# Performance work log

Hardware: AMD Instinct MI355X
Metric: run time of the kernel (lower is better)

The kernel has to match this reference:

```python
import jax, jax.numpy as jnp
import numpy as np

NUM_HEADS = 8
NUM_LEVELS = 4
NUM_POINTS = 4


def setup_inputs() -> dict:
    key = jax.random.key(0)
    kq, kp, kv, k1, k2, k3, k4 = jax.random.split(key, 7)
    B, Q, C = 4, 4096, 256
    M, L, P = NUM_HEADS, NUM_LEVELS, NUM_POINTS
    shapes_np = np.array([[128, 128], [64, 64], [32, 32], [16, 16]], dtype=np.int32)
    sizes = shapes_np[:, 0] * shapes_np[:, 1]
    N = int(sizes.sum())  # 21760
    level_index = jnp.asarray(np.concatenate([[0], np.cumsum(sizes)[:-1]]).astype(np.int32))
    q = jax.random.normal(kq, (B, Q, C), jnp.float32)
    p = jax.random.uniform(kp, (B, Q, L, 2), jnp.float32)  # normalized ref points
    v = jax.random.normal(kv, (B, N, C), jnp.float32)
    # proj_offset bias: radial grid init from reset_parameters()
    t = np.arange(M, dtype=np.float32) * (2.0 * np.pi / M)
    grid = np.stack([np.cos(t), np.sin(t)], -1)
    grid = grid / np.abs(grid).max(-1, keepdims=True)
    grid = np.tile(grid[:, None, None, :], (1, L, P, 1)) * np.arange(1, P + 1, dtype=np.float32)[None, None, :, None]
    b_off = jnp.asarray(grid.reshape(-1))
    s = 1.0 / np.sqrt(C).astype(np.float32)
    W_off = jax.random.normal(k1, (C, M * L * P * 2), jnp.float32) * 0.01
    W_attn = jax.random.normal(k2, (C, M * L * P), jnp.float32) * s
    b_attn = jnp.zeros((M * L * P,), jnp.float32)
    W_val = jax.random.normal(k3, (C, C), jnp.float32) * s
    b_val = jnp.zeros((C,), jnp.float32)
    W_out = jax.random.normal(k4, (C, C), jnp.float32) * s
    b_out = jnp.zeros((C,), jnp.float32)
    return {"q": q, "p": p, "v": v, "shapes": jnp.asarray(shapes_np), "level_index": level_index,
            "W_off": W_off, "b_off": b_off, "W_attn": W_attn, "b_attn": b_attn,
            "W_val": W_val, "b_val": b_val, "W_out": W_out, "b_out": b_out}


def _ms_deform_attn(q, p, v, shapes, level_index, W_off, b_off, W_attn, b_attn, W_val, b_val, W_out, b_out):
    B, Q, C = q.shape
    M, L, P = NUM_HEADS, NUM_LEVELS, NUM_POINTS
    D = C // M
    N = v.shape[1]
    # value projection -> [B, M, N, D] (head-major for gather)
    v_p = (v @ W_val + b_val).reshape(B, N, M, D).transpose(0, 2, 1, 3)
    # attention weights, softmax over L*P (classic MSDeformAttn kernel contract)
    attn = jax.nn.softmax((q @ W_attn + b_attn).reshape(B, Q, M, L * P), axis=-1)
    attn = attn.reshape(B, Q, M, L, P)
    # sampling locations (P==2 reference-point branch)
    off = (q @ W_off + b_off).reshape(B, Q, M, L, P, 2)
    norm = jnp.stack([shapes[:, 1], shapes[:, 0]], -1).astype(jnp.float32)  # (W, H) per level
    loc = p[:, :, None, :, None, :] + off / norm[None, None, None, :, None, :]  # [B,Q,M,L,P,2]

    out = jnp.zeros((B, M, Q, D), jnp.float32)
    for l in range(L):
        Hf = shapes[l, 0].astype(jnp.float32)
        Wf = shapes[l, 1].astype(jnp.float32)
        Hi = shapes[l, 0]
        Wi = shapes[l, 1]
        base = level_index[l]
        # grid_sample(align_corners=False) convention: pixel = loc*size - 0.5
        x = loc[:, :, :, l, :, 0] * Wf - 0.5  # [B,Q,M,P]
        y = loc[:, :, :, l, :, 1] * Hf - 0.5
        x0 = jnp.floor(x)
        y0 = jnp.floor(y)
        lx, ly = x - x0, y - y0
        x0i = x0.astype(jnp.int32)
        y0i = y0.astype(jnp.int32)

        def corner(xi, yi, w):
            valid = (xi >= 0) & (xi < Wi) & (yi >= 0) & (yi < Hi)
            idx = base + jnp.clip(yi, 0, Hi - 1) * Wi + jnp.clip(xi, 0, Wi - 1)  # [B,Q,M,P]
            idx = idx.transpose(0, 2, 1, 3).reshape(B, M, Q * P)
            g = jnp.take_along_axis(v_p, idx[..., None], axis=2).reshape(B, M, Q, P, D)
            wv = (w * valid.astype(w.dtype)).transpose(0, 2, 1, 3)[..., None]  # [B,M,Q,P,1]
            return g * wv

        samp = (corner(x0i, y0i, (1 - lx) * (1 - ly))
                + corner(x0i + 1, y0i, lx * (1 - ly))
                + corner(x0i, y0i + 1, (1 - lx) * ly)
                + corner(x0i + 1, y0i + 1, lx * ly))  # [B,M,Q,P,D]
        a_l = attn[:, :, :, l, :].transpose(0, 2, 1, 3)  # [B,M,Q,P]
        out = out + jnp.einsum('bmqpd,bmqp->bmqd', samp, a_l)

    out = out.transpose(0, 2, 1, 3).reshape(B, Q, M * D)
    return out @ W_out + b_out


def reference(q, p, v, shapes, level_index, W_off, b_off, W_attn, b_attn, W_val, b_val, W_out, b_out):
    return _ms_deform_attn(q, p, v, shapes, level_index, W_off, b_off, W_attn, b_attn, W_val, b_val, W_out, b_out)
```

## Files before the change

### kernel.cpp

```cpp
#include <hip/hip_runtime.h>
#include <cstddef>

#define BB 4
#define QQ 4096
#define MM 8
#define NN 21760

typedef __bf16 bf16_8 __attribute__((ext_vector_type(8)));
typedef __bf16 bf16_4 __attribute__((ext_vector_type(4)));
typedef float  floatx4 __attribute__((ext_vector_type(4)));

__global__ __launch_bounds__(256) void prep_weights(
    const float* __restrict__ Wv, const float* __restrict__ Wa,
    const float* __restrict__ Wo, const float* __restrict__ Wu,
    const float* __restrict__ ba, const float* __restrict__ bo,
    __bf16* __restrict__ Wt, float* __restrict__ biasq)
{
    const int gid = blockIdx.x * 256 + threadIdx.x;
    if (gid < 65536) {
        const int n = gid >> 8, k = gid & 255;
        Wt[gid] = (__bf16)Wv[k * 256 + n];
    } else if (gid < 163840) {
        const int o = gid - 65536;
        const int n = o >> 8, k = o & 255;
        Wt[gid] = (__bf16)(n < 128 ? Wa[k * 128 + n] : Wo[k * 256 + (n - 128)]);
    } else if (gid < 229376) {
        const int o = gid - 163840;
        const int n = o >> 8, k = o & 255;
        Wt[gid] = (__bf16)Wu[k * 256 + n];
    } else if (gid < 229760) {
        const int j = gid - 229376;
        biasq[j] = (j < 128) ? ba[j] : bo[j - 128];
    }
}

template<typename AT, int NCOLS, int MODE>
__global__ __launch_bounds__(256) void gemm_k64(
    const AT* __restrict__ A,
    const __bf16* __restrict__ Bt,
    const float* __restrict__ bias,
    void* __restrict__ Cout,
    int tokens, int ldc)
{
    constexpr int NJ  = NCOLS / 64;
    constexpr int BCH = NCOLS / 32;

    const int z    = blockIdx.z;
    const int row0 = blockIdx.y * 64;
    const AT* Ab = A + (size_t)z * tokens * 256;

    __shared__ __bf16 As[64][68];
    __shared__ __bf16 Bs[NCOLS][68];

    const int tid  = threadIdx.x;
    const int lane = tid & 63;
    const int wave = tid >> 6;
    const int quad = lane >> 4;
    const int l16  = lane & 15;
    const int wave_n = wave * (NCOLS / 4);

    floatx4 acc[4][NJ] = {};

    for (int k0 = 0; k0 < 256; k0 += 64) {
        float4 a4[4];
        bf16_8 a8[2];
        if (sizeof(AT) == 4) {
            const float* Af = (const float*)Ab;
            #pragma unroll
            for (int c = 0; c < 4; ++c) {
                const int cid = c * 256 + tid;
                const int r   = cid >> 4;
                const int kc  = (cid & 15) * 4;
                a4[c] = *(const float4*)(Af + (size_t)(row0 + r) * 256 + k0 + kc);
            }
        } else {
            const __bf16* Ah = (const __bf16*)Ab;
            #pragma unroll
            for (int c = 0; c < 2; ++c) {
                const int cid = c * 256 + tid;
                const int r   = cid >> 3;
                const int kc  = (cid & 7) * 8;
                a8[c] = *(const bf16_8*)(Ah + (size_t)(row0 + r) * 256 + k0 + kc);
            }
        }
        bf16_8 b8[BCH];
        #pragma unroll
        for (int c = 0; c < BCH; ++c) {
            const int cid = c * 256 + tid;
            const int n   = cid >> 3;
            const int kc  = (cid & 7) * 8;
            b8[c] = *(const bf16_8*)(Bt + (size_t)n * 256 + k0 + kc);
        }
        if (sizeof(AT) == 4) {
            #pragma unroll
            for (int c = 0; c < 4; ++c) {
                const int cid = c * 256 + tid;
                const int r   = cid >> 4;
                const int kc  = (cid & 15) * 4;
                bf16_4 w;
                w[0] = (__bf16)a4[c].x; w[1] = (__bf16)a4[c].y;
                w[2] = (__bf16)a4[c].z; w[3] = (__bf16)a4[c].w;
                *(bf16_4*)&As[r][kc] = w;
            }
        } else {
            #pragma unroll
            for (int c = 0; c < 2; ++c) {
                const int cid = c * 256 + tid;
                const int r   = cid >> 3;
                const int kc  = (cid & 7) * 8;
                *(bf16_8*)&As[r][kc] = a8[c];
            }
        }
        #pragma unroll
        for (int c = 0; c < BCH; ++c) {
            const int cid = c * 256 + tid;
            const int n   = cid >> 3;
            const int kc  = (cid & 7) * 8;
            *(bf16_8*)&Bs[n][kc] = b8[c];
        }
        __syncthreads();
        #pragma unroll
        for (int h = 0; h < 2; ++h) {
            bf16_8 af[4], bfr[NJ];
            #pragma unroll
            for (int i = 0; i < 4; ++i)
                af[i] = *(const bf16_8*)&As[i * 16 + l16][h * 32 + quad * 8];
            #pragma unroll
            for (int j = 0; j < NJ; ++j)
                bfr[j] = *(const bf16_8*)&Bs[wave_n + j * 16 + l16][h * 32 + quad * 8];
            #pragma unroll
            for (int i = 0; i < 4; ++i)
                #pragma unroll
                for (int j = 0; j < NJ; ++j)
                    acc[i][j] = __builtin_amdgcn_mfma_f32_16x16x32_bf16(af[i], bfr[j], acc[i][j], 0, 0, 0);
        }
        __syncthreads();
    }

    #pragma unroll
    for (int j = 0; j < NJ; ++j) {
        const int col = wave_n + j * 16 + l16;
        const float bc = bias[col];
        #pragma unroll
        for (int i = 0; i < 4; ++i) {
            #pragma unroll
            for (int r = 0; r < 4; ++r) {
                const int row = row0 + i * 16 + quad * 4 + r;
                const float val = acc[i][j][r] + bc;
                if (MODE == 0) {
                    ((float*)Cout)[((size_t)z * tokens + row) * ldc + col] = val;
                } else {
                    const int m = col >> 5, dd = col & 31;
                    ((__bf16*)Cout)[(((size_t)z * 8 + m) * NN + row) * 32 + dd] = (__bf16)val;
                }
            }
        }
    }
}

__device__ __forceinline__ float bflo(unsigned u) { return __uint_as_float(u << 16); }
__device__ __forceinline__ float bfhi(unsigned u) { return __uint_as_float(u & 0xffff0000u); }

__global__ __launch_bounds__(512) void sampler(
    const __bf16* __restrict__ vp,
    const float* __restrict__ gqp,
    const float* __restrict__ pref,
    __bf16* __restrict__ mid)
{
    const int t    = threadIdx.x;
    const int m    = t >> 6;
    const int lane = t & 63;
    const int s    = lane >> 2;
    const int c    = lane & 3;
    const int l    = s >> 2;
    const int bq   = blockIdx.x;
    const int b    = bq >> 12;

    const int   Hi = 128 >> l;
    const float Hf = (float)Hi;
    const int   base = (l == 0) ? 0 : (l == 1) ? 16384 : (l == 2) ? 20480 : 21504;

    const float logit = gqp[(size_t)bq * 384 + m * 16 + s];
    const float e = __expf(logit);
    float sum = e;
    #pragma unroll
    for (int k = 4; k < 64; k <<= 1) sum += __shfl_xor(sum, k, 64);
    const float a = e * __builtin_amdgcn_rcpf(sum);

    const float2 off = *(const float2*)(gqp + (size_t)bq * 384 + 128 + (m * 16 + s) * 2);
    const float2 pr  = *(const float2*)(pref + (size_t)bq * 8 + l * 2);

    const float x = fmaf(pr.x, Hf, off.x - 0.5f);
    const float y = fmaf(pr.y, Hf, off.y - 0.5f);
    const float x0f = floorf(x), y0f = floorf(y);
    const float lx = x - x0f, ly = y - y0f;
    const int x0 = (int)x0f, y0 = (int)y0f;
    const int cx0 = min(max(x0, 0), Hi - 1), cx1 = min(max(x0 + 1, 0), Hi - 1);
    const int cy0 = min(max(y0, 0), Hi - 1), cy1 = min(max(y0 + 1, 0), Hi - 1);
    const bool vx0 = (x0 >= 0) && (x0 < Hi), vx1 = (x0 + 1 >= 0) && (x0 + 1 < Hi);
    const bool vy0 = (y0 >= 0) && (y0 < Hi), vy1 = (y0 + 1 >= 0) && (y0 + 1 < Hi);
    const float w00 = a * (1.f - lx) * (1.f - ly) * ((vx0 && vy0) ? 1.f : 0.f);
    const float w10 = a * lx * (1.f - ly) * ((vx1 && vy0) ? 1.f : 0.f);
    const float w01 = a * (1.f - lx) * ly * ((vx0 && vy1) ? 1.f : 0.f);
    const float w11 = a * lx * ly * ((vx1 && vy1) ? 1.f : 0.f);

    const __bf16* vbase = vp + ((size_t)b * 8 + m) * NN * 32;
    const uint4 u00 = *((const uint4*)(vbase + (size_t)(base + cy0 * Hi + cx0) * 32) + c);
    const uint4 u10 = *((const uint4*)(vbase + (size_t)(base + cy0 * Hi + cx1) * 32) + c);
    const uint4 u01 = *((const uint4*)(vbase + (size_t)(base + cy1 * Hi + cx0) * 32) + c);
    const uint4 u11 = *((const uint4*)(vbase + (size_t)(base + cy1 * Hi + cx1) * 32) + c);

    float f[8];
    f[0] = w00*bflo(u00.x) + w10*bflo(u10.x) + w01*bflo(u01.x) + w11*bflo(u11.x);
    f[1] = w00*bfhi(u00.x) + w10*bfhi(u10.x) + w01*bfhi(u01.x) + w11*bfhi(u11.x);
    f[2] = w00*bflo(u00.y) + w10*bflo(u10.y) + w01*bflo(u01.y) + w11*bflo(u11.y);
    f[3] = w00*bfhi(u00.y) + w10*bfhi(u10.y) + w01*bfhi(u01.y) + w11*bfhi(u11.y);
    f[4] = w00*bflo(u00.z) + w10*bflo(u10.z) + w01*bflo(u01.z) + w11*bflo(u11.z);
    f[5] = w00*bfhi(u00.z) + w10*bfhi(u10.z) + w01*bfhi(u01.z) + w11*bfhi(u11.z);
    f[6] = w00*bflo(u00.w) + w10*bflo(u10.w) + w01*bflo(u01.w) + w11*bflo(u11.w);
    f[7] = w00*bfhi(u00.w) + w10*bfhi(u10.w) + w01*bfhi(u01.w) + w11*bfhi(u11.w);

    const int b2 = (lane >> 2) & 1, b3 = (lane >> 3) & 1, b4 = (lane >> 4) & 1;
    #pragma unroll
    for (int j = 0; j < 4; ++j) {
        const float sel  = b2 ? f[j] : f[j + 4];
        const float recv = __shfl_xor(sel, 4, 64);
        f[j] = (b2 ? f[j + 4] : f[j]) + recv;
    }
    #pragma unroll
    for (int j = 0; j < 2; ++j) {
        const float sel  = b3 ? f[j] : f[j + 2];
        const float recv = __shfl_xor(sel, 8, 64);
        f[j] = (b3 ? f[j + 2] : f[j]) + recv;
    }
    {
        const float sel  = b4 ? f[0] : f[1];
        const float recv = __shfl_xor(sel, 16, 64);
        f[0] = (b4 ? f[1] : f[0]) + recv;
    }
    f[0] += __shfl_xor(f[0], 32, 64);

    if (!(lane & 32)) {
        const int chan = (c << 3) | (b2 << 2) | (b3 << 1) | b4;
        mid[(size_t)bq * 256 + m * 32 + chan] = (__bf16)f[0];
    }
}

extern "C" void kernel_launch(void* const* d_in, const int* in_sizes, int n_in,
                              void* d_out, int out_size, void* d_ws, size_t ws_size,
                              hipStream_t stream) {
    const float* q      = (const float*)d_in[0];
    const float* p      = (const float*)d_in[1];
    const float* v      = (const float*)d_in[2];
    const float* W_off  = (const float*)d_in[5];
    const float* b_off  = (const float*)d_in[6];
    const float* W_attn = (const float*)d_in[7];
    const float* b_attn = (const float*)d_in[8];
    const float* W_val  = (const float*)d_in[9];
    const float* b_val  = (const float*)d_in[10];
    const float* W_out  = (const float*)d_in[11];
    const float* b_out  = (const float*)d_in[12];
    float* out = (float*)d_out;

    float*  gqp   = (float*)d_ws;
    float*  biasq = gqp + (size_t)16384 * 384;
    __bf16* mid   = (__bf16*)(biasq + 384);
    __bf16* vpb   = mid + (size_t)16384 * 256;
    __bf16* Wt    = vpb + (size_t)BB * 8 * NN * 32;
    __bf16* Wt_val  = Wt;
    __bf16* Wt_attn = Wt + 65536;
    __bf16* Wt_off  = Wt + 65536 + 32768;
    __bf16* Wt_out  = Wt + 163840;

    prep_weights<<<898, 256, 0, stream>>>(W_val, W_attn, W_off, W_out, b_attn, b_off, Wt, biasq);

    {
        dim3 grid(1, NN / 64, BB);
        gemm_k64<float, 256, 1><<<grid, 256, 0, stream>>>(v, Wt_val, b_val, vpb, NN, 0);
    }
    {
        dim3 grid(1, (BB * QQ) / 64, 1);
        gemm_k64<float, 128, 0><<<grid, 256, 0, stream>>>(q, Wt_attn, biasq, gqp, BB * QQ, 384);
    }
    {
        dim3 grid(1, (BB * QQ) / 64, 1);
        gemm_k64<float, 256, 0><<<grid, 256, 0, stream>>>(q, Wt_off, biasq + 128, gqp + 128, BB * QQ, 384);
    }
    sampler<<<BB * QQ, 512, 0, stream>>>(vpb, gqp, p, mid);
    {
        dim3 grid(1, (BB * QQ) / 64, 1);
        gemm_k64<__bf16, 256, 0><<<grid, 256, 0, stream>>>(mid, Wt_out, b_out, out, BB * QQ, 256);
    }
}
```

Baseline: 258.1 us.

## Restructure GEMM: weights direct from global, double-buffered A tile, swapped MFMA operands

The GEMM kernel no longer stages the weight matrix through shared memory. Each wave loads its weight fragments straight from global/L2, and the activation tile is double-buffered in LDS so the next K-slice loads while the current one is multiplied. This drops one barrier per iteration. MFMA operands are swapped so that accumulators hold 4 consecutive output columns per lane, which lets the epilogue use vectorized float4/bf16x4 stores and a vector bias load. The trade-off is more redundant global weight traffic per block and higher register use for the prefetched tiles.

```diff
diff --git a/kernel.cpp b/kernel.cpp
--- a/kernel.cpp
+++ b/kernel.cpp
@@ -35,124 +35,145 @@
 }
 
 template<typename AT, int NCOLS, int MODE>
-__global__ __launch_bounds__(256) void gemm_k64(
+__global__ __launch_bounds__(256) void gemm_bd(
     const AT* __restrict__ A,
-    const __bf16* __restrict__ Bt,
+    const __bf16* __restrict__ Wn,
     const float* __restrict__ bias,
     void* __restrict__ Cout,
     int tokens, int ldc)
 {
-    constexpr int NJ  = NCOLS / 64;
-    constexpr int BCH = NCOLS / 32;
-
+    constexpr int NJ = NCOLS / 64;
     const int z    = blockIdx.z;
     const int row0 = blockIdx.y * 64;
     const AT* Ab = A + (size_t)z * tokens * 256;
 
-    __shared__ __bf16 As[64][68];
-    __shared__ __bf16 Bs[NCOLS][68];
+    __shared__ __bf16 As[2][64][68];
 
     const int tid  = threadIdx.x;
     const int lane = tid & 63;
     const int wave = tid >> 6;
     const int quad = lane >> 4;
     const int l16  = lane & 15;
-    const int wave_n = wave * (NCOLS / 4);
-
-    floatx4 acc[4][NJ] = {};
-
-    for (int k0 = 0; k0 < 256; k0 += 64) {
-        float4 a4[4];
-        bf16_8 a8[2];
-        if (sizeof(AT) == 4) {
-            const float* Af = (const float*)Ab;
-            #pragma unroll
-            for (int c = 0; c < 4; ++c) {
-                const int cid = c * 256 + tid;
-                const int r   = cid >> 4;
-                const int kc  = (cid & 15) * 4;
-                a4[c] = *(const float4*)(Af + (size_t)(row0 + r) * 256 + k0 + kc);
+    const int wave_f = wave * (NCOLS / 4);
+
+    floatx4 acc[NJ][4] = {};
+
+    if (sizeof(AT) == 4) {
+        const float* Af = (const float*)Ab;
+        #pragma unroll
+        for (int c = 0; c < 4; ++c) {
+            const int cid = c * 256 + tid;
+            const int r   = cid >> 4;
+            const int kc  = (cid & 15) * 4;
+            const float4 av = *(const float4*)(Af + (size_t)(row0 + r) * 256 + kc);
+            bf16_4 w;
+            w[0] = (__bf16)av.x; w[1] = (__bf16)av.y; w[2] = (__bf16)av.z; w[3] = (__bf16)av.w;
+            *(bf16_4*)&As[0][r][kc] = w;
+        }
+    } else {
+        const __bf16* Ah = (const __bf16*)Ab;
+        #pragma unroll
+        for (int c = 0; c < 2; ++c) {
+            const int cid = c * 256 + tid;
+            const int r   = cid >> 3;
+            const int kc  = (cid & 7) * 8;
+            *(bf16_8*)&As[0][r][kc] = *(const bf16_8*)(Ah + (size_t)(row0 + r) * 256 + kc);
+        }
+    }
+    __syncthreads();
+
+    for (int i = 0; i < 4; ++i) {
+        const int k0  = i * 64;
+        const int cur = i & 1;
+
+        float4 a4[4]; bf16_8 a8[2];
+        if (i < 3) {
+            if (sizeof(AT) == 4) {
+                const float* Af = (const float*)Ab;
+                #pragma unroll
+                for (int c = 0; c < 4; ++c) {
+                    const int cid = c * 256 + tid;
+                    const int r   = cid >> 4;
+                    const int kc  = (cid & 15) * 4;
+                    a4[c] = *(const float4*)(Af + (size_t)(row0 + r) * 256 + k0 + 64 + kc);
+                }
+            } else {
+                const __bf16* Ah = (const __bf16*)Ab;
+                #pragma unroll
+                for (int c = 0; c < 2; ++c) {
+                    const int cid = c * 256 + tid;
+                    const int r   = cid >> 3;
+                    const int kc  = (cid & 7) * 8;
+                    a8[c] = *(const bf16_8*)(Ah + (size_t)(row0 + r) * 256 + k0 + 64 + kc);
+                }
             }
-        } else {
-            const __bf16* Ah = (const __bf16*)Ab;
-            #pragma unroll
-            for (int c = 0; c < 2; ++c) {
-                const int cid = c * 256 + tid;
-                const int r   = cid >> 3;
-                const int kc  = (cid & 7) * 8;
-                a8[c] = *(const bf16_8*)(Ah + (size_t)(row0 + r) * 256 + k0 + kc);
-            }
-        }
-        bf16_8 b8[BCH];
-        #pragma unroll
-        for (int c = 0; c < BCH; ++c) {
-            const int cid = c * 256 + tid;
-            const int n   = cid >> 3;
-            const int kc  = (cid & 7) * 8;
-            b8[c] = *(const bf16_8*)(Bt + (size_t)n * 256 + k0 + kc);
-        }
-        if (sizeof(AT) == 4) {
-            #pragma unroll
-            for (int c = 0; c < 4; ++c) {
-                const int cid = c * 256 + tid;
-                const int r   = cid >> 4;
-                const int kc  = (cid & 15) * 4;
-                bf16_4 w;
-                w[0] = (__bf16)a4[c].x; w[1] = (__bf16)a4[c].y;
-                w[2] = (__bf16)a4[c].z; w[3] = (__bf16)a4[c].w;
-                *(bf16_4*)&As[r][kc] = w;
-            }
-        } else {
-            #pragma unroll
-            for (int c = 0; c < 2; ++c) {
-                const int cid = c * 256 + tid;
-                const int r   = cid >> 3;
-                const int kc  = (cid & 7) * 8;
-                *(bf16_8*)&As[r][kc] = a8[c];
-            }
-        }
-        #pragma unroll
-        for (int c = 0; c < BCH; ++c) {
-            const int cid = c * 256 + tid;
-            const int n   = cid >> 3;
-            const int kc  = (cid & 7) * 8;
-            *(bf16_8*)&Bs[n][kc] = b8[c];
-        }
-        __syncthreads();
-        #pragma unroll
-        for (int h = 0; h < 2; ++h) {
-            bf16_8 af[4], bfr[NJ];
-            #pragma unroll
-            for (int i = 0; i < 4; ++i)
-                af[i] = *(const bf16_8*)&As[i * 16 + l16][h * 32 + quad * 8];
+        }
+
+        bf16_8 wf[2][NJ];
+        #pragma unroll
+        for (int h = 0; h < 2; ++h)
             #pragma unroll
             for (int j = 0; j < NJ; ++j)
-                bfr[j] = *(const bf16_8*)&Bs[wave_n + j * 16 + l16][h * 32 + quad * 8];
+                wf[h][j] = *(const bf16_8*)(Wn + (size_t)(wave_f + j * 16 + l16) * 256
+                                             + k0 + h * 32 + quad * 8);
+
+        #pragma unroll
+        for (int h = 0; h < 2; ++h) {
+            bf16_8 af[4];
             #pragma unroll
-            for (int i = 0; i < 4; ++i)
-                #pragma unroll
-                for (int j = 0; j < NJ; ++j)
-                    acc[i][j] = __builtin_amdgcn_mfma_f32_16x16x32_bf16(af[i], bfr[j], acc[i][j], 0, 0, 0);
-        }
-        __syncthreads();
+            for (int it = 0; it < 4; ++it)
+                af[it] = *(const bf16_8*)&As[cur][it * 16 + l16][h * 32 + quad * 8];
+            #pragma unroll
+            for (int j = 0; j < NJ; ++j)
+                #pragma unroll
+                for (int it = 0; it < 4; ++it)
+                    acc[j][it] = __builtin_amdgcn_mfma_f32_16x16x32_bf16(wf[h][j], af[it], acc[j][it], 0, 0, 0);
+        }
+
+        if (i < 3) {
+            if (sizeof(AT) == 4) {
+                #pragma unroll
+                for (int c = 0; c < 4; ++c) {
+                    const int cid = c * 256 + tid;
+                    const int r   = cid >> 4;
+                    const int kc  = (cid & 15) * 4;
+                    bf16_4 w;
+                    w[0] = (__bf16)a4[c].x; w[1] = (__bf16)a4[c].y;
+                    w[2] = (__bf16)a4[c].z; w[3] = (__bf16)a4[c].w;
+                    *(bf16_4*)&As[cur ^ 1][r][kc] = w;
+                }
+            } else {
+                #pragma unroll
+                for (int c = 0; c < 2; ++c) {
+                    const int cid = c * 256 + tid;
+                    const int r   = cid >> 3;
+                    const int kc  = (cid & 7) * 8;
+                    *(bf16_8*)&As[cur ^ 1][r][kc] = a8[c];
+                }
+            }
+            __syncthreads();
+        }
     }
 
     #pragma unroll
     for (int j = 0; j < NJ; ++j) {
-        const int col = wave_n + j * 16 + l16;
-        const float bc = bias[col];
-        #pragma unroll
-        for (int i = 0; i < 4; ++i) {
-            #pragma unroll
-            for (int r = 0; r < 4; ++r) {
-                const int row = row0 + i * 16 + quad * 4 + r;
-                const float val = acc[i][j][r] + bc;
-                if (MODE == 0) {
-                    ((float*)Cout)[((size_t)z * tokens + row) * ldc + col] = val;
-                } else {
-                    const int m = col >> 5, dd = col & 31;
-                    ((__bf16*)Cout)[(((size_t)z * 8 + m) * NN + row) * 32 + dd] = (__bf16)val;
-                }
+        const int n0 = wave_f + j * 16 + quad * 4;
+        const float4 b4 = *(const float4*)(bias + n0);
+        #pragma unroll
+        for (int it = 0; it < 4; ++it) {
+            const int token = row0 + it * 16 + l16;
+            const float v0 = acc[j][it][0] + b4.x;
+            const float v1 = acc[j][it][1] + b4.y;
+            const float v2 = acc[j][it][2] + b4.z;
+            const float v3 = acc[j][it][3] + b4.w;
+            if (MODE == 0) {
+                float4 o; o.x = v0; o.y = v1; o.z = v2; o.w = v3;
+                *(float4*)((float*)Cout + ((size_t)z * tokens + token) * ldc + n0) = o;
+            } else {
+                const int mh = n0 >> 5, dd = n0 & 31;
+                bf16_4 ob;
+                ob[0] = (__bf16)v0; ob[1] = (__bf16)v1; ob[2] = (__bf16)v2; ob[3] = (__bf16)v3;
+                *(bf16_4*)((__bf16*)Cout + (((size_t)z * 8 + mh) * NN + token) * 32 + dd) = ob;
             }
         }
     }
@@ -220,7 +241,7 @@
     f[6] = w00*bflo(u00.w) + w10*bflo(u10.w) + w01*bflo(u01.w) + w11*bflo(u11.w);
     f[7] = w00*bfhi(u00.w) + w10*bfhi(u10.w) + w01*bfhi(u01.w) + w11*bfhi(u11.w);
 
-    const int b2 = (lane >> 2) & 1, b3 = (lane >> 3) & 1, b4 = (lane >> 4) & 1;
+    const int b2 = (lane >> 2) & 1, b3 = (lane >> 3) & 1, b4i = (lane >> 4) & 1;
     #pragma unroll
     for (int j = 0; j < 4; ++j) {
         const float sel  = b2 ? f[j] : f[j + 4];
@@ -234,14 +255,14 @@
         f[j] = (b3 ? f[j + 2] : f[j]) + recv;
     }
     {
-        const float sel  = b4 ? f[0] : f[1];
+        const float sel  = b4i ? f[0] : f[1];
         const float recv = __shfl_xor(sel, 16, 64);
-        f[0] = (b4 ? f[1] : f[0]) + recv;
+        f[0] = (b4i ? f[1] : f[0]) + recv;
     }
     f[0] += __shfl_xor(f[0], 32, 64);
 
     if (!(lane & 32)) {
-        const int chan = (c << 3) | (b2 << 2) | (b3 << 1) | b4;
+        const int chan = (c << 3) | (b2 << 2) | (b3 << 1) | b4i;
         mid[(size_t)bq * 256 + m * 32 + chan] = (__bf16)f[0];
     }
 }
@@ -276,19 +297,19 @@
 
     {
         dim3 grid(1, NN / 64, BB);
-        gemm_k64<float, 256, 1><<<grid, 256, 0, stream>>>(v, Wt_val, b_val, vpb, NN, 0);
+        gemm_bd<float, 256, 1><<<grid, 256, 0, stream>>>(v, Wt_val, b_val, vpb, NN, 0);
     }
     {
         dim3 grid(1, (BB * QQ) / 64, 1);
-        gemm_k64<float, 128, 0><<<grid, 256, 0, stream>>>(q, Wt_attn, biasq, gqp, BB * QQ, 384);
+        gemm_bd<float, 128, 0><<<grid, 256, 0, stream>>>(q, Wt_attn, biasq, gqp, BB * QQ, 384);
     }
     {
         dim3 grid(1, (BB * QQ) / 64, 1);
-        gemm_k64<float, 256, 0><<<grid, 256, 0, stream>>>(q, Wt_off, biasq + 128, gqp + 128, BB * QQ, 384);
+        gemm_bd<float, 256, 0><<<grid, 256, 0, stream>>>(q, Wt_off, biasq + 128, gqp + 128, BB * QQ, 384);
     }
     sampler<<<BB * QQ, 512, 0, stream>>>(vpb, gqp, p, mid);
     {
         dim3 grid(1, (BB * QQ) / 64, 1);
-        gemm_k64<__bf16, 256, 0><<<grid, 256, 0, stream>>>(mid, Wt_out, b_out, out, BB * QQ, 256);
+        gemm_bd<__bf16, 256, 0><<<grid, 256, 0, stream>>>(mid, Wt_out, b_out, out, BB * QQ, 256);
     }
 }
```

Measured after the change: 263.3 us. +2.0%, slower.
